# Kernel tuning notes

Hardware: AMD Instinct MI355X
Metric: run time of the kernel (lower is better)

## Reference

```python
import jax, jax.numpy as jnp
import numpy as np
from math import factorial

STENCIL = [5, 5]
ORDERS = [2, 2]
NDIMS = 2
N_ITER = 5
PAD = STENCIL[0] // 2  # 2


def _fd_coeffs_1d(size, order):
    # Centered finite-difference coefficients: sum_i c_i * off_i^k = k! * delta_{k,order}
    off = np.arange(size) - size // 2
    V = np.vander(off, increasing=True).T  # V[k, i] = off_i^k
    b = np.zeros(size)
    b[order] = factorial(order)
    return np.linalg.solve(V, b)


def _build_coeffs():
    coeffs = np.zeros((NDIMS,) + tuple(STENCIL))
    for d in range(NDIMS):
        c = _fd_coeffs_1d(STENCIL[d], ORDERS[d])
        idx = [s // 2 for s in STENCIL]
        idx[d] = slice(None)
        coeffs[(d,) + tuple(idx)] = c
    center = tuple(s // 2 for s in STENCIL)
    diag = coeffs[(slice(None),) + center].copy()  # [ndims], diagonal stencil values
    coeffs[(slice(None),) + center] = 0.0          # LU part (diagonal removed)
    return coeffs, diag

_LU_np, _DIAG_np = _build_coeffs()
LU_COEFFS = jnp.asarray(_LU_np, dtype=jnp.float32)      # [ndims, 5, 5]
DIAG_COEFFS = jnp.asarray(_DIAG_np, dtype=jnp.float32)  # [ndims]
ORDERS_ARR = jnp.asarray(ORDERS, dtype=jnp.float32)


def setup_inputs() -> dict:
    key = jax.random.key(0)
    k1, k2, k3 = jax.random.split(key, 3)
    B, H, W = 16, 1024, 1024
    current_guess = jax.random.normal(k1, (B, 1, H, W), dtype=jnp.float32)
    rhses = jax.random.normal(k2, (B, 1, H, W), dtype=jnp.float32)
    # grid spacings: positive, realistic magnitudes (avoid near-zero -> huge 1/dx)
    dx = jax.random.uniform(k3, (B, NDIMS), dtype=jnp.float32, minval=0.005, maxval=0.02)
    return {"current_guess": current_guess, "rhses": rhses, "dx": dx}


def _conv_one(x, k):
    # x: [H, W]; k: [5, 5] -> VALID conv, output [H-4, W-4]
    out = jax.lax.conv_general_dilated(
        x[None, None], k[:, :, None, None], (1, 1), 'VALID',
        dimension_numbers=('NCHW', 'HWIO', 'NCHW'))
    return out[0, 0]


def reference(current_guess, rhses, dx):
    B, _, H, W = current_guess.shape
    dxp = jnp.power(1.0 / dx, ORDERS_ARR[None, :])            # [B, ndims]
    kernels = jnp.einsum('dhw,bd->bhw', LU_COEFFS, dxp)       # [B, 5, 5] per-sample LU kernel
    d_inv = 1.0 / jnp.einsum('bd,d->b', dxp, DIAG_COEFFS)     # [B]
    rhs_int = rhses[:, 0, PAD:-PAD, PAD:-PAD]                 # [B, H-4, W-4]
    # boundary mask: 1 on the PAD-wide frame, 0 in the interior
    mask = jnp.ones((H, W), dtype=current_guess.dtype).at[PAD:-PAD, PAD:-PAD].set(0.0)

    def step(g):
        cr = jax.vmap(_conv_one)(g[:, 0], kernels)            # [B, H-4, W-4]
        interior = d_inv[:, None, None] * (rhs_int - cr)
        new = jnp.pad(interior, ((0, 0), (PAD, PAD), (PAD, PAD)))
        return (new + g[:, 0] * mask)[:, None]                # keep boundary from g

    g = current_guess
    for _ in range(N_ITER):
        g = step(g)
    return g
```

## Files before the change

kernel.cpp:

```cpp
#include <hip/hip_runtime.h>


#define HH 1024
#define WW 1024
#define NB 16
#define GX 10
#define GY 24
#define TX 104
#define TY 44
#define HALO 12
#define TWX 128
#define NOCT 8
#define NTHREADS 256
#define NITER 5
#define NBLK (GX * GY * NB)
#define NXCD 8
#define CHUNK (NBLK / NXCD)
#define XB (NOCT * 4 * TWX)
#define FZOFF (2 * XB)

struct Coef { float sH1, sH2, sW1, sW2; };

__device__ __forceinline__ float4 ld4(const float* p) { return *(const float4*)p; }
__device__ __forceinline__ void st4(float* p, float4 v) { *(float4*)p = v; }

__device__ __forceinline__ float dpp_shr1(float x) {
    return __int_as_float(__builtin_amdgcn_update_dpp(
        0, __float_as_int(x), 0x138 , 0xf, 0xf, true));
}
__device__ __forceinline__ float dpp_shl1(float x) {
    return __int_as_float(__builtin_amdgcn_update_dpp(
        0, __float_as_int(x), 0x130 , 0xf, 0xf, true));
}

__device__ __forceinline__ float4 ld4g(const float* img, int gy, int gxl) {
    gy = gy < 0 ? 0 : (gy > HH - 1 ? HH - 1 : gy);
    const float* row = img + (size_t)gy * WW;
    if (gxl >= 0 && gxl <= WW - 4) return ld4(row + gxl);
    int xa = gxl + 0; xa = xa < 0 ? 0 : (xa > WW - 1 ? WW - 1 : xa);
    int xb = gxl + 1; xb = xb < 0 ? 0 : (xb > WW - 1 ? WW - 1 : xb);
    int xc = gxl + 2; xc = xc < 0 ? 0 : (xc > WW - 1 ? WW - 1 : xc);
    int xd = gxl + 3; xd = xd < 0 ? 0 : (xd > WW - 1 ? WW - 1 : xd);
    return make_float4(row[xa], row[xb], row[xc], row[xd]);
}

template <bool EDGE>
__device__ __forceinline__ float4 row_update(
    const float4 a2, const float4 a1, const float4 ct, const float4 b1, const float4 b2,
    const float4 rv, const Coef cf, const int gy, const int gx0)
{
    const float hmx = dpp_shr1(ct.z);
    const float hmy = dpp_shr1(ct.w);
    const float hpx = dpp_shl1(ct.x);
    const float hpy = dpp_shl1(ct.y);
    const float A2[4] = {a2.x, a2.y, a2.z, a2.w};
    const float A1[4] = {a1.x, a1.y, a1.z, a1.w};
    const float CT[4] = {ct.x, ct.y, ct.z, ct.w};
    const float B1[4] = {b1.x, b1.y, b1.z, b1.w};
    const float B2[4] = {b2.x, b2.y, b2.z, b2.w};
    const float RV[4] = {rv.x, rv.y, rv.z, rv.w};
    const float cc[8] = {hmx, hmy, ct.x, ct.y, ct.z, ct.w, hpx, hpy};
    const bool rowok = (gy >= 2) && (gy < HH - 2);
    float o[4];
#pragma unroll
    for (int k = 0; k < 4; ++k) {
        float v = RV[k];
        v = fmaf(cf.sH2, A2[k] + B2[k], v);
        v = fmaf(cf.sH1, A1[k] + B1[k], v);
        v = fmaf(cf.sW2, cc[k] + cc[k + 4], v);
        v = fmaf(cf.sW1, cc[k + 1] + cc[k + 3], v);
        if (EDGE) {
            const int gx = gx0 + k;
            const bool ok = rowok && (gx >= 2) && (gx < WW - 2);
            v = ok ? v : CT[k];
        }
        o[k] = v;
    }
    return make_float4(o[0], o[1], o[2], o[3]);
}

template <bool EDGE>
__device__ __forceinline__ void sweeps(
    float* lds, float4 (&f)[8], float4 (&rv)[8], const Coef cf,
    const int oct, const int c, const int gyb, const int gx0,
    float* ob, const int x0, const int y0)
{
    const float* pmu = (oct > 0) ? lds + ((oct - 1) * 4 + 2) * TWX + c
                                 : lds + FZOFF + 0 * TWX + c;
    const float* ppd = (oct < NOCT - 1) ? lds + ((oct + 1) * 4 + 0) * TWX + c
                                        : lds + FZOFF + 2 * TWX + c;
    const int mo = (oct > 0) ? XB : 0;
    const int po = (oct < NOCT - 1) ? XB : 0;
    float* wr = lds + (oct * 4) * TWX + c;

#pragma unroll
    for (int it = 0; it < NITER; ++it) {
        const int ro = (it & 1) ? mo : 0;
        const int rp = (it & 1) ? po : 0;
        const int wo = (it & 1) ? 0 : XB;

        const float4 fm2 = ld4(pmu + ro);
        const float4 fm1 = ld4(pmu + ro + TWX);
        float4 o0 = row_update<EDGE>(fm2, fm1, f[0], f[1], f[2], rv[0], cf, gyb + 0, gx0);
        float4 o1 = row_update<EDGE>(fm1, f[0], f[1], f[2], f[3], rv[1], cf, gyb + 1, gx0);
        float4 o2 = row_update<EDGE>(f[0], f[1], f[2], f[3], f[4], rv[2], cf, gyb + 2, gx0);
        f[0] = o0;
        float4 o3 = row_update<EDGE>(f[1], f[2], f[3], f[4], f[5], rv[3], cf, gyb + 3, gx0);
        f[1] = o1;
        float4 o4 = row_update<EDGE>(f[2], f[3], f[4], f[5], f[6], rv[4], cf, gyb + 4, gx0);
        f[2] = o2;
        float4 o5 = row_update<EDGE>(f[3], f[4], f[5], f[6], f[7], rv[5], cf, gyb + 5, gx0);
        f[3] = o3;
        const float4 fp0 = ld4(ppd + rp);
        const float4 fp1 = ld4(ppd + rp + TWX);
        float4 o6 = row_update<EDGE>(f[4], f[5], f[6], f[7], fp0, rv[6], cf, gyb + 6, gx0);
        f[4] = o4;
        float4 o7 = row_update<EDGE>(f[5], f[6], f[7], fp0, fp1, rv[7], cf, gyb + 7, gx0);
        f[5] = o5;

        if (it < NITER - 1) {
            st4(wr + wo + 0 * TWX, o0);
            st4(wr + wo + 1 * TWX, o1);
            st4(wr + wo + 2 * TWX, o6);
            st4(wr + wo + 3 * TWX, o7);
            f[6] = o6; f[7] = o7;
            __syncthreads();
        } else {
            const int gxl = x0 + c - HALO;
            if ((c >= HALO) && (c < HALO + TX) && (gxl <= WW - 4)) {
                const int trow0 = gyb - (y0 - HALO);
                float* obase = ob + (size_t)(y0 + trow0 - HALO) * WW + gxl;
                const int gylim = HH - (y0 + trow0 - HALO);
#define ST_ROW(J, OJ) \
                if (trow0 + (J) >= HALO && trow0 + (J) < HALO + TY && (J) < gylim) \
                    st4(obase + (size_t)(J) * WW, OJ);
                ST_ROW(0, o0) ST_ROW(1, o1) ST_ROW(2, o2) ST_ROW(3, o3)
                ST_ROW(4, o4) ST_ROW(5, o5) ST_ROW(6, o6) ST_ROW(7, o7)
#undef ST_ROW
            }
        }
    }
}

__global__ __launch_bounds__(NTHREADS, 2) void jacobi_fused(
    const float* __restrict__ g0, const float* __restrict__ rhs,
    const float* __restrict__ dx, float* __restrict__ out)
{
    __shared__ __align__(16) float lds[2 * XB + 4 * TWX];

    const int tid = (int)threadIdx.x;

    const int h = (int)blockIdx.x + GX * ((int)blockIdx.y + GY * (int)blockIdx.z);
    const int l = (h & (NXCD - 1)) * CHUNK + (h >> 3);
    const int tx = l % GX;
    const int t2 = l / GX;
    const int ty = t2 % GY;
    const int b  = t2 / GY;
    const int x0 = tx * TX, y0 = ty * TY;

    const float* gb = g0 + (size_t)b * HH * WW;
    const float* rb = rhs + (size_t)b * HH * WW;
    float* ob = out + (size_t)b * HH * WW;

    const float t0 = 1.0f / dx[2 * b + 0], t1 = 1.0f / dx[2 * b + 1];
    const float p0 = t0 * t0, p1 = t1 * t1;
    const float d_inv = 1.0f / (-2.5f * (p0 + p1));
    Coef cf;
    cf.sH1 = -d_inv * (4.0f / 3.0f) * p0;
    cf.sH2 = -d_inv * (-1.0f / 12.0f) * p0;
    cf.sW1 = -d_inv * (4.0f / 3.0f) * p1;
    cf.sW2 = -d_inv * (-1.0f / 12.0f) * p1;

    const int oct = tid >> 5;
    const int cg  = tid & 31;
    const int c   = 4 * cg;
    const int gx0 = x0 - HALO + c;
    const int trow0 = 2 + 8 * oct;
    const int gyb = y0 - HALO + trow0;

    float4 f[8], rvv[8];
#pragma unroll
    for (int j = 0; j < 8; ++j) {
        f[j] = ld4g(gb, gyb + j, gx0);
        const float4 v = ld4g(rb, gyb + j, gx0);
        rvv[j] = make_float4(d_inv * v.x, d_inv * v.y, d_inv * v.z, d_inv * v.w);
    }

    st4(&lds[(oct * 4 + 0) * TWX + c], f[0]);
    st4(&lds[(oct * 4 + 1) * TWX + c], f[1]);
    st4(&lds[(oct * 4 + 2) * TWX + c], f[6]);
    st4(&lds[(oct * 4 + 3) * TWX + c], f[7]);
    if (oct == 0) {
        st4(&lds[FZOFF + 0 * TWX + c], ld4g(gb, y0 - HALO + 0, gx0));
        st4(&lds[FZOFF + 1 * TWX + c], ld4g(gb, y0 - HALO + 1, gx0));
    } else if (oct == NOCT - 1) {
        st4(&lds[FZOFF + 2 * TWX + c], ld4g(gb, y0 - HALO + 66, gx0));
        st4(&lds[FZOFF + 3 * TWX + c], ld4g(gb, y0 - HALO + 67, gx0));
    }
    __syncthreads();

    const bool interior = (x0 - HALO >= 2) && (x0 + TX + HALO <= WW - 2) &&
                          (y0 - HALO >= 2) && (y0 + TY + HALO <= HH - 2);
    if (interior)
        sweeps<false>(lds, f, rvv, cf, oct, c, gyb, gx0, ob, x0, y0);
    else
        sweeps<true >(lds, f, rvv, cf, oct, c, gyb, gx0, ob, x0, y0);
}

extern "C" void kernel_launch(void* const* d_in, const int* in_sizes, int n_in,
                              void* d_out, int out_size, void* d_ws, size_t ws_size,
                              hipStream_t stream) {
    const float* g0  = (const float*)d_in[0];
    const float* rhs = (const float*)d_in[1];
    const float* dx  = (const float*)d_in[2];
    float* out = (float*)d_out;

    dim3 grid(GX, GY, NB), block(NTHREADS);
    jacobi_fused<<<grid, block, 0, stream>>>(g0, rhs, dx, out);
}
```

Measured before the change: 212.7 us.

## Shrink vertical halo to 10 rows and keep frozen boundary rows in registers

The vertical halo shrinks from 12 to 10 rows, which is the minimum for 5 Jacobi sweeps with a radius-2 stencil. This lets each tile produce 48 output rows instead of 44, so fewer tiles (22 instead of 24 in y) are needed and less halo is recomputed. The frozen outermost two rows are now kept in registers of the edge octets rather than in a separate LDS region, which trims LDS size and removes the per-iteration offset selection. The cost is that the last tile row overhangs the image bottom and relies on clamped loads and guarded stores.

```diff
diff --git a/kernel.cpp b/kernel.cpp
--- a/kernel.cpp
+++ b/kernel.cpp
@@ -5,11 +5,13 @@
 #define WW 1024
 #define NB 16
 #define GX 10
-#define GY 24
+#define GY 22
 #define TX 104
-#define TY 44
-#define HALO 12
+#define TY 48
+#define HALOX 12
+#define HALOY 10
 #define TWX 128
+#define TWY 68
 #define NOCT 8
 #define NTHREADS 256
 #define NITER 5
@@ -17,7 +19,6 @@
 #define NXCD 8
 #define CHUNK (NBLK / NXCD)
 #define XB (NOCT * 4 * TWX)
-#define FZOFF (2 * XB)
 
 struct Coef { float sH1, sH2, sW1, sW2; };
 
@@ -81,26 +82,23 @@
 
 template <bool EDGE>
 __device__ __forceinline__ void sweeps(
-    float* lds, float4 (&f)[8], float4 (&rv)[8], const Coef cf,
+    float* lds, float4 (&f)[8], float4 (&rv)[8],
+    const float4 fz0, const float4 fz1, const Coef cf,
     const int oct, const int c, const int gyb, const int gx0,
     float* ob, const int x0, const int y0)
 {
-    const float* pmu = (oct > 0) ? lds + ((oct - 1) * 4 + 2) * TWX + c
-                                 : lds + FZOFF + 0 * TWX + c;
-    const float* ppd = (oct < NOCT - 1) ? lds + ((oct + 1) * 4 + 0) * TWX + c
-                                        : lds + FZOFF + 2 * TWX + c;
-    const int mo = (oct > 0) ? XB : 0;
-    const int po = (oct < NOCT - 1) ? XB : 0;
+    const float* pmu = lds + ((oct > 0 ? oct - 1 : 0) * 4 + 2) * TWX + c;
+    const float* ppd = lds + ((oct < NOCT - 1 ? oct + 1 : oct) * 4 + 0) * TWX + c;
     float* wr = lds + (oct * 4) * TWX + c;
 
 #pragma unroll
     for (int it = 0; it < NITER; ++it) {
-        const int ro = (it & 1) ? mo : 0;
-        const int rp = (it & 1) ? po : 0;
+        const int ro = (it & 1) ? XB : 0;
         const int wo = (it & 1) ? 0 : XB;
 
-        const float4 fm2 = ld4(pmu + ro);
-        const float4 fm1 = ld4(pmu + ro + TWX);
+        float4 fm2, fm1;
+        if (oct > 0) { fm2 = ld4(pmu + ro); fm1 = ld4(pmu + ro + TWX); }
+        else         { fm2 = fz0; fm1 = fz1; }
         float4 o0 = row_update<EDGE>(fm2, fm1, f[0], f[1], f[2], rv[0], cf, gyb + 0, gx0);
         float4 o1 = row_update<EDGE>(fm1, f[0], f[1], f[2], f[3], rv[1], cf, gyb + 1, gx0);
         float4 o2 = row_update<EDGE>(f[0], f[1], f[2], f[3], f[4], rv[2], cf, gyb + 2, gx0);
@@ -111,8 +109,9 @@
         f[2] = o2;
         float4 o5 = row_update<EDGE>(f[3], f[4], f[5], f[6], f[7], rv[5], cf, gyb + 5, gx0);
         f[3] = o3;
-        const float4 fp0 = ld4(ppd + rp);
-        const float4 fp1 = ld4(ppd + rp + TWX);
+        float4 fp0, fp1;
+        if (oct < NOCT - 1) { fp0 = ld4(ppd + ro); fp1 = ld4(ppd + ro + TWX); }
+        else                { fp0 = fz0; fp1 = fz1; }
         float4 o6 = row_update<EDGE>(f[4], f[5], f[6], f[7], fp0, rv[6], cf, gyb + 6, gx0);
         f[4] = o4;
         float4 o7 = row_update<EDGE>(f[5], f[6], f[7], fp0, fp1, rv[7], cf, gyb + 7, gx0);
@@ -126,14 +125,14 @@
             f[6] = o6; f[7] = o7;
             __syncthreads();
         } else {
-            const int gxl = x0 + c - HALO;
-            if ((c >= HALO) && (c < HALO + TX) && (gxl <= WW - 4)) {
-                const int trow0 = gyb - (y0 - HALO);
-                float* obase = ob + (size_t)(y0 + trow0 - HALO) * WW + gxl;
-                const int gylim = HH - (y0 + trow0 - HALO);
+            const int gxl = x0 + c - HALOX;
+            if ((c >= HALOX) && (c < HALOX + TX) && (gxl <= WW - 4)) {
+                const int trow0 = gyb - (y0 - HALOY);
+                float* obase = ob + (ptrdiff_t)gyb * WW + gxl;
+                const int gylim = HH - gyb;
 #define ST_ROW(J, OJ) \
-                if (trow0 + (J) >= HALO && trow0 + (J) < HALO + TY && (J) < gylim) \
-                    st4(obase + (size_t)(J) * WW, OJ);
+                if (trow0 + (J) >= HALOY && trow0 + (J) < HALOY + TY && (J) < gylim) \
+                    st4(obase + (ptrdiff_t)(J) * WW, OJ);
                 ST_ROW(0, o0) ST_ROW(1, o1) ST_ROW(2, o2) ST_ROW(3, o3)
                 ST_ROW(4, o4) ST_ROW(5, o5) ST_ROW(6, o6) ST_ROW(7, o7)
 #undef ST_ROW
@@ -146,7 +145,7 @@
     const float* __restrict__ g0, const float* __restrict__ rhs,
     const float* __restrict__ dx, float* __restrict__ out)
 {
-    __shared__ __align__(16) float lds[2 * XB + 4 * TWX];
+    __shared__ __align__(16) float lds[2 * XB];
 
     const int tid = (int)threadIdx.x;
 
@@ -174,9 +173,9 @@
     const int oct = tid >> 5;
     const int cg  = tid & 31;
     const int c   = 4 * cg;
-    const int gx0 = x0 - HALO + c;
+    const int gx0 = x0 - HALOX + c;
     const int trow0 = 2 + 8 * oct;
-    const int gyb = y0 - HALO + trow0;
+    const int gyb = y0 - HALOY + trow0;
 
     float4 f[8], rvv[8];
 #pragma unroll
@@ -186,25 +185,27 @@
         rvv[j] = make_float4(d_inv * v.x, d_inv * v.y, d_inv * v.z, d_inv * v.w);
     }
 
+    float4 fz0 = {0,0,0,0}, fz1 = {0,0,0,0};
+    if (oct == 0) {
+        fz0 = ld4g(gb, y0 - HALOY + 0, gx0);
+        fz1 = ld4g(gb, y0 - HALOY + 1, gx0);
+    } else if (oct == NOCT - 1) {
+        fz0 = ld4g(gb, y0 - HALOY + TWY - 2, gx0);
+        fz1 = ld4g(gb, y0 - HALOY + TWY - 1, gx0);
+    }
+
     st4(&lds[(oct * 4 + 0) * TWX + c], f[0]);
     st4(&lds[(oct * 4 + 1) * TWX + c], f[1]);
     st4(&lds[(oct * 4 + 2) * TWX + c], f[6]);
     st4(&lds[(oct * 4 + 3) * TWX + c], f[7]);
-    if (oct == 0) {
-        st4(&lds[FZOFF + 0 * TWX + c], ld4g(gb, y0 - HALO + 0, gx0));
-        st4(&lds[FZOFF + 1 * TWX + c], ld4g(gb, y0 - HALO + 1, gx0));
-    } else if (oct == NOCT - 1) {
-        st4(&lds[FZOFF + 2 * TWX + c], ld4g(gb, y0 - HALO + 66, gx0));
-        st4(&lds[FZOFF + 3 * TWX + c], ld4g(gb, y0 - HALO + 67, gx0));
-    }
     __syncthreads();
 
-    const bool interior = (x0 - HALO >= 2) && (x0 + TX + HALO <= WW - 2) &&
-                          (y0 - HALO >= 2) && (y0 + TY + HALO <= HH - 2);
+    const bool interior = (x0 - HALOX >= 2) && (x0 - HALOX + TWX <= WW - 2) &&
+                          (y0 - HALOY >= 2) && (y0 - HALOY + TWY <= HH - 2);
     if (interior)
-        sweeps<false>(lds, f, rvv, cf, oct, c, gyb, gx0, ob, x0, y0);
+        sweeps<false>(lds, f, rvv, fz0, fz1, cf, oct, c, gyb, gx0, ob, x0, y0);
     else
-        sweeps<true >(lds, f, rvv, cf, oct, c, gyb, gx0, ob, x0, y0);
+        sweeps<true >(lds, f, rvv, fz0, fz1, cf, oct, c, gyb, gx0, ob, x0, y0);
 }
 
 extern "C" void kernel_launch(void* const* d_in, const int* in_sizes, int n_in,
```

New measurement: 202.1 us. 5.0% less time.
